# Optimization experiments

Measured on AMD Instinct MI355X. Metric: run time of the kernel, lower is better.

## Reference

```python
import jax, jax.numpy as jnp
import numpy as np

D = 256
H = 8
DH = D // H
N_NODES = 2048
N_EDGES = 4096
NEG = -10000.0
LN_EPS = 1e-5


def _layernorm(x, g, b):
    mu = jnp.mean(x, axis=-1, keepdims=True)
    var = jnp.var(x, axis=-1, keepdims=True)
    return (x - mu) * jax.lax.rsqrt(var + LN_EPS) * g + b


def setup_inputs() -> dict:
    key = jax.random.key(0)
    ks = jax.random.split(key, 20)
    s = 0.05
    x = jax.random.normal(ks[0], (N_NODES, D), jnp.float32)
    edge_index = jax.random.randint(ks[1], (2, N_EDGES), 0, N_NODES)
    edge_attr = jax.random.normal(ks[2], (N_EDGES, D), jnp.float32)
    edge_masks = jax.random.bernoulli(ks[3], 0.95, (N_EDGES, N_EDGES))
    return {
        "x": x,
        "edge_index": edge_index,
        "edge_attr": edge_attr,
        "edge_masks": edge_masks,
        # message MLP: Linear(3d, d) -> LeakyReLU(0.2) -> Linear(d, d)
        "W1": jax.random.normal(ks[4], (D, 3 * D), jnp.float32) * s,
        "b1": jnp.zeros((D,), jnp.float32),
        "W2": jax.random.normal(ks[5], (D, D), jnp.float32) * s,
        "b2": jnp.zeros((D,), jnp.float32),
        # MultiheadAttention params
        "in_proj_w": jax.random.normal(ks[6], (3 * D, D), jnp.float32) * s,
        "in_proj_b": jnp.zeros((3 * D,), jnp.float32),
        "out_w": jax.random.normal(ks[7], (D, D), jnp.float32) * s,
        "out_b": jnp.zeros((D,), jnp.float32),
        # GraphConv root weight + bias
        "root": jax.random.normal(ks[8], (D, D), jnp.float32) * s,
        "bias_p": jnp.zeros((D,), jnp.float32),
        # LayerNorms + residual linear
        "ln1_g": jnp.ones((D,), jnp.float32),
        "ln1_b": jnp.zeros((D,), jnp.float32),
        "ln2_g": jnp.ones((D,), jnp.float32),
        "ln2_b": jnp.zeros((D,), jnp.float32),
        "lin_w": jax.random.normal(ks[9], (D, D), jnp.float32) * s,
        "lin_b": jnp.zeros((D,), jnp.float32),
    }


def reference(x, edge_index, edge_attr, edge_masks,
              W1, b1, W2, b2,
              in_proj_w, in_proj_b, out_w, out_b,
              root, bias_p, ln1_g, ln1_b, ln2_g, ln2_b, lin_w, lin_b):
    # --- message: gather endpoints, concat with edge features, MLP ---
    x_j = x[edge_index[0]]            # source [E, d]
    x_i = x[edge_index[1]]            # target [E, d]
    h = jnp.concatenate([x_i, x_j, edge_attr], axis=1)          # [E, 3d]
    h = jax.nn.leaky_relu(h @ W1.T + b1, negative_slope=0.2)
    h = h @ W2.T + b2                                            # [E, d]

    # --- MultiheadAttention over edges (L=E, batch=1), eval mode ---
    qkv = h @ in_proj_w.T + in_proj_b                            # [E, 3d]
    q, k, v = jnp.split(qkv, 3, axis=1)
    q = q.reshape(N_EDGES, H, DH).transpose(1, 0, 2)             # [H, E, dh]
    k = k.reshape(N_EDGES, H, DH).transpose(1, 0, 2)
    v = v.reshape(N_EDGES, H, DH).transpose(1, 0, 2)
    scores = jnp.einsum('hed,hfd->hef', q, k) / np.sqrt(DH)      # [H, E, E]
    add_mask = jnp.where(edge_masks, 0.0, NEG).astype(scores.dtype)
    attn = jax.nn.softmax(scores + add_mask[None], axis=-1)
    o = jnp.einsum('hef,hfd->hed', attn, v)                      # [H, E, dh]
    o = o.transpose(1, 0, 2).reshape(N_EDGES, D)
    msg = o @ out_w.T + out_b                                    # [E, d]

    # --- scatter-add aggregation to target nodes + update ---
    aggr = jax.ops.segment_sum(msg, edge_index[1], num_segments=N_NODES)
    out = aggr + x @ root + bias_p                               # [N, d]

    # --- graph_block: norm1 -> residual linear -> norm2 ---
    y = _layernorm(out, ln1_g, ln1_b)
    y = _layernorm(y + (y @ lin_w.T + lin_b), ln2_g, ln2_b)
    return y
```

## Files before the change

### kernel.cpp

```cpp
#include <hip/hip_runtime.h>
#include <hip/hip_bf16.h>
#include <cstdint>

#define D_   256
#define E_   4096
#define NN_  2048

typedef float f32x4_t __attribute__((ext_vector_type(4)));
typedef short bf16x8_t __attribute__((ext_vector_type(8)));
typedef short bf16x4_t __attribute__((ext_vector_type(4)));

__device__ inline short f2bf(float f) {
    union { float fv; unsigned u; } v; v.fv = f;
    unsigned r = v.u + 0x7fffu + ((v.u >> 16) & 1u);
    return (short)(r >> 16);
}

__device__ inline unsigned cvtpk_bf16(float lo, float hi) {
    unsigned r;
    asm("v_cvt_pk_bf16_f32 %0, %1, %2" : "=v"(r) : "v"(lo), "v"(hi));
    return r;
}

__device__ inline float hw_exp2(float x) {
    float r;
    asm("v_exp_f32 %0, %1" : "=v"(r) : "v"(x));
    return r;
}

template<int ACT, bool GATHER, bool SCATTER, bool HASADD, bool ABF16, int OUT>
__global__ __launch_bounds__(256)
void mgemm_k(const void* __restrict__ A, const float* __restrict__ Bm,
             const float* __restrict__ bias, const float* __restrict__ addsrc,
             void* __restrict__ C, short* __restrict__ vtb,
             int M, int N, int K,
             const int* __restrict__ ei0, const int* __restrict__ ei1,
             const float* __restrict__ x, const float* __restrict__ eattr,
             float qsc)
{
    __shared__ char lds[16384];
    const int tid = threadIdx.x;
    const int w = tid >> 6, l = tid & 63;
    const int g = l >> 4, ln = l & 15;
    const int wr = w >> 1, wc = w & 1;
    const int m0 = blockIdx.x * 64, n0 = blockIdx.y * 64;

    const int srow = tid >> 2;
    const int sck  = (tid & 3) * 8;
    const int sswz = (srow & 7) << 4;
    int gi1 = 0, gi0 = 0;
    if (GATHER) { gi1 = ei1[m0 + srow]; gi0 = ei0[m0 + srow]; }

    f32x4_t acc[2][2];
    #pragma unroll
    for (int m = 0; m < 2; m++)
        #pragma unroll
        for (int n = 0; n < 2; n++)
            acc[m][n] = f32x4_t{0.f, 0.f, 0.f, 0.f};

    const int nt = K >> 5;
    float4 ga0, ga1, gb0, gb1;
    bf16x8_t gab;

    auto loadG = [&](int kk) {
        const int cb = kk + sck;
        if (ABF16) {
            gab = *(const bf16x8_t*)((const short*)A + (size_t)(m0 + srow) * K + cb);
        } else {
            const float* src;
            if (GATHER) {
                if (cb < 256)      src = x + (size_t)gi1 * 256 + cb;
                else if (cb < 512) src = x + (size_t)gi0 * 256 + (cb - 256);
                else               src = eattr + (size_t)(m0 + srow) * 256 + (cb - 512);
            } else {
                src = (const float*)A + (size_t)(m0 + srow) * K + cb;
            }
            ga0 = *(const float4*)src;
            ga1 = *(const float4*)(src + 4);
        }
        const float* bsrc = Bm + (size_t)(n0 + srow) * K + cb;
        gb0 = *(const float4*)bsrc;
        gb1 = *(const float4*)(bsrc + 4);
    };
    auto writeS = [&](int buf) {
        const int off = (srow*64 + sck*2) ^ sswz;
        if (ABF16) {
            *(bf16x8_t*)(lds + buf*4096 + off) = gab;
        } else {
            uint4 pa;
            pa.x = cvtpk_bf16(ga0.x, ga0.y); pa.y = cvtpk_bf16(ga0.z, ga0.w);
            pa.z = cvtpk_bf16(ga1.x, ga1.y); pa.w = cvtpk_bf16(ga1.z, ga1.w);
            *(uint4*)(lds + buf*4096 + off) = pa;
        }
        uint4 pb;
        pb.x = cvtpk_bf16(gb0.x, gb0.y); pb.y = cvtpk_bf16(gb0.z, gb0.w);
        pb.z = cvtpk_bf16(gb1.x, gb1.y); pb.w = cvtpk_bf16(gb1.z, gb1.w);
        *(uint4*)(lds + 8192 + buf*4096 + off) = pb;
    };

    loadG(0);
    writeS(0);
    __syncthreads();
    int cur = 0;
    for (int t = 0; t < nt; ++t) {
        if (t + 1 < nt) loadG((t + 1) << 5);
        bf16x8_t af[2], bfr[2];
        #pragma unroll
        for (int m = 0; m < 2; m++) {
            const int row = wr*32 + m*16 + ln;
            af[m] = *(const bf16x8_t*)(lds + cur*4096 + ((row*64 + g*16) ^ ((row&7)<<4)));
        }
        #pragma unroll
        for (int n = 0; n < 2; n++) {
            const int row = wc*32 + n*16 + ln;
            bfr[n] = *(const bf16x8_t*)(lds + 8192 + cur*4096 + ((row*64 + g*16) ^ ((row&7)<<4)));
        }
        #pragma unroll
        for (int m = 0; m < 2; m++)
            #pragma unroll
            for (int n = 0; n < 2; n++)
                acc[m][n] = __builtin_amdgcn_mfma_f32_16x16x32_bf16(af[m], bfr[n], acc[m][n], 0, 0, 0);
        if (t + 1 < nt) writeS(cur ^ 1);
        __syncthreads();
        cur ^= 1;
    }

    #pragma unroll
    for (int m = 0; m < 2; m++) {
        #pragma unroll
        for (int n = 0; n < 2; n++) {
            const int col = n0 + wc*32 + n*16 + ln;
            const float bv = bias[col];
            const int row0 = m0 + wr*32 + m*16 + g*4;
            float pv[4];
            #pragma unroll
            for (int r = 0; r < 4; r++) {
                float v = acc[m][n][r] + bv;
                if (ACT == 1) v = v > 0.f ? v : 0.2f * v;
                if (HASADD) v += addsrc[(size_t)(row0 + r) * N + col];
                pv[r] = v;
            }
            if (SCATTER) {
                #pragma unroll
                for (int r = 0; r < 4; r++)
                    atomicAdd(&((float*)C)[(size_t)ei1[row0 + r] * 256 + col], pv[r]);
            } else if (OUT == 0) {
                #pragma unroll
                for (int r = 0; r < 4; r++)
                    ((float*)C)[(size_t)(row0 + r) * N + col] = pv[r];
            } else if (OUT == 1) {
                #pragma unroll
                for (int r = 0; r < 4; r++)
                    ((short*)C)[(size_t)(row0 + r) * N + col] =
                        f2bf((col < 256) ? pv[r] * qsc : pv[r]);
            } else {
                if (col < 512) {
                    #pragma unroll
                    for (int r = 0; r < 4; r++)
                        ((short*)C)[(size_t)(row0 + r) * 768 + col] =
                            f2bf((col < 256) ? pv[r] * qsc : pv[r]);
                } else {
                    const int hd = (col - 512) >> 5, d = (col - 512) & 31;
                    bf16x4_t pk;
                    #pragma unroll
                    for (int r = 0; r < 4; r++) pk[r] = f2bf(pv[r]);
                    *(bf16x4_t*)(vtb + (size_t)hd*131072 + (size_t)d*4096 + row0) = pk;
                }
            }
        }
    }
}

__global__ __launch_bounds__(256)
void prep_k(const int* __restrict__ mraw, unsigned int* __restrict__ pm,
            const float* __restrict__ root, float* __restrict__ rootT,
            float* __restrict__ aggr)
{
    __shared__ float T[64][65];
    const int bid = blockIdx.x;
    if (bid < 2048) {
        const int t = bid * 256 + threadIdx.x;
        aggr[t] = 0.f;
        const int row = t >> 7, wb = t & 127;
        unsigned int bits = 0;
        const uint4* p = (const uint4*)(mraw + (size_t)row * 4096 + wb * 32);
        #pragma unroll
        for (int g = 0; g < 8; g++) {
            const uint4 v = p[g];
            if (v.x) bits |= 1u << (g*4+0);
            if (v.y) bits |= 1u << (g*4+1);
            if (v.z) bits |= 1u << (g*4+2);
            if (v.w) bits |= 1u << (g*4+3);
        }
        pm[t] = bits;
    } else {
        const int bt = bid - 2048;
        const int m0 = (bt >> 2) * 64, n0 = (bt & 3) * 64;
        const int r = threadIdx.x >> 6, c = threadIdx.x & 63;
        #pragma unroll
        for (int i = 0; i < 16; i++)
            T[r + i*4][c] = root[(size_t)(m0 + r + i*4) * 256 + n0 + c];
        __syncthreads();
        #pragma unroll
        for (int i = 0; i < 16; i++)
            rootT[(size_t)(n0 + r + i*4) * 256 + m0 + c] = T[c][r + i*4];
    }
}

__global__ __launch_bounds__(512, 4)
void attn_k(const short* __restrict__ qkvb, const short* __restrict__ vt,
            const unsigned int* __restrict__ pmask, float* __restrict__ o)
{
    __shared__ char lds[49152];
    const int tid = threadIdx.x;
    const int w2 = tid >> 6, l = tid & 63;
    const int g = l >> 4, ln = l & 15;
    const int gi = w2 >> 2, wq = w2 & 3;
    const int head = blockIdx.x >> 6;
    const int q0 = (blockIdx.x & 63) * 64;
    const int qa = q0 + wq * 16 + ln;

    const bf16x8_t qf = *(const bf16x8_t*)(qkvb + (size_t)qa*768 + head*32 + g*8);

    f32x4_t oT0 = {0.f,0.f,0.f,0.f};
    f32x4_t oT1 = {0.f,0.f,0.f,0.f};
    float lsum = 0.f;

    const int st = tid & 255;
    const int skey = st >> 2, sc = st & 3;
    const int sd = st >> 3, skc = st & 7;
    const short* kgp = qkvb + 256 + head*32 + sc*8;
    const short* vgp = vt + (size_t)head*131072 + (size_t)sd*4096 + skc*8;
    char* Kg = lds + gi*8192;
    char* Vg = lds + 16384 + gi*8192;
    char* Pw = lds + 32768 + w2*2048;
    const unsigned int* mrow = pmask + (size_t)qa*128;
    const int kswz = (skey & 7) << 4, vswz = (sd & 7) << 4;
    const int pswz = (ln & 7) << 4;

    uint2 mwc;
    {
        const int k0 = gi * 64;
        const bf16x8_t kv = *(const bf16x8_t*)(kgp + (size_t)(k0 + skey)*768);
        *(bf16x8_t*)(Kg + ((skey*64 + sc*16) ^ kswz)) = kv;
        const bf16x8_t vv = *(const bf16x8_t*)(vgp + k0);
        *(bf16x8_t*)(Vg + ((sd*128 + skc*16) ^ vswz)) = vv;
        mwc = *(const uint2*)(mrow + gi*2);
    }

    for (int i = 0; i < 32; ++i) {
        __syncthreads();
        const int cur = i & 1;
        const int tt = 2*i + gi;
        uint2 mwn;
        if (i < 31) {
            const int k0n = (tt + 2) * 64;
            const bf16x8_t kv = *(const bf16x8_t*)(kgp + (size_t)(k0n + skey)*768);
            *(bf16x8_t*)(Kg + (cur^1)*4096 + ((skey*64 + sc*16) ^ kswz)) = kv;
            const bf16x8_t vv = *(const bf16x8_t*)(vgp + k0n);
            *(bf16x8_t*)(Vg + (cur^1)*4096 + ((sd*128 + skc*16) ^ vswz)) = vv;
            mwn = *(const uint2*)(mrow + (tt + 2)*2);
        }
        char* Kb = Kg + cur*4096;
        char* Vb = Vg + cur*4096;

        f32x4_t s[4];
        __builtin_amdgcn_s_setprio(1);
        #pragma unroll
        for (int kt = 0; kt < 4; kt++) {
            const int key = kt*16 + ln;
            const bf16x8_t kf = *(const bf16x8_t*)(Kb + ((key*64 + g*16) ^ ((key & 7) << 4)));
            f32x4_t z = {0.f,0.f,0.f,0.f};
            s[kt] = __builtin_amdgcn_mfma_f32_16x16x32_bf16(kf, qf, z, 0, 0, 0);
        }
        __builtin_amdgcn_s_setprio(0);

        #pragma unroll
        for (int kt = 0; kt < 4; kt++) {
            const unsigned word = (kt < 2) ? mwc.x : mwc.y;
            float p[4];
            #pragma unroll
            for (int r = 0; r < 4; r++) {
                const float e = hw_exp2(s[kt][r] - 17.312340490667562f);
                p[r] = ((word >> ((kt & 1)*16 + g*4 + r)) & 1u) ? e : 0.f;
            }
            lsum += (p[0] + p[1]) + (p[2] + p[3]);
            uint2 pk;
            pk.x = cvtpk_bf16(p[0], p[1]);
            pk.y = cvtpk_bf16(p[2], p[3]);
            *(uint2*)(Pw + ((ln*128 + kt*32 + g*8) ^ pswz)) = pk;
        }

        __builtin_amdgcn_s_setprio(1);
        #pragma unroll
        for (int kh = 0; kh < 2; kh++) {
            const bf16x8_t pf = *(const bf16x8_t*)(Pw + ((ln*128 + kh*64 + g*16) ^ pswz));
            const bf16x8_t vf0 = *(const bf16x8_t*)(Vb + ((ln*128 + kh*64 + g*16) ^ pswz));
            const bf16x8_t vf1 = *(const bf16x8_t*)(Vb + (((16+ln)*128 + kh*64 + g*16) ^ pswz));
            oT0 = __builtin_amdgcn_mfma_f32_16x16x32_bf16(vf0, pf, oT0, 0, 0, 0);
            oT1 = __builtin_amdgcn_mfma_f32_16x16x32_bf16(vf1, pf, oT1, 0, 0, 0);
        }
        __builtin_amdgcn_s_setprio(0);
        mwc = mwn;
    }

    __syncthreads();
    *(f32x4_t*)(lds + w2*2048 + l*32)      = oT0;
    *(f32x4_t*)(lds + w2*2048 + l*32 + 16) = oT1;
    ((float*)(lds + 16384))[w2*64 + l] = lsum;
    __syncthreads();
    if (gi == 0) {
        const int pw = w2 + 4;
        const f32x4_t b0 = *(const f32x4_t*)(lds + pw*2048 + l*32);
        const f32x4_t b1 = *(const f32x4_t*)(lds + pw*2048 + l*32 + 16);
        const float lp = ((const float*)(lds + 16384))[pw*64 + l];
        oT0 += b0; oT1 += b1;
        lsum += lp;
        lsum += __shfl_xor(lsum, 16);
        lsum += __shfl_xor(lsum, 32);
        const float inv = 1.0f / fmaxf(lsum, 1e-37f);
        float* op = o + (size_t)qa * 256 + head*32;
        float4 v0 = {oT0[0]*inv, oT0[1]*inv, oT0[2]*inv, oT0[3]*inv};
        float4 v1 = {oT1[0]*inv, oT1[1]*inv, oT1[2]*inv, oT1[3]*inv};
        *(float4*)(op + g*4) = v0;
        *(float4*)(op + 16 + g*4) = v1;
    }
}

__global__ __launch_bounds__(256)
void ln_k(const float* __restrict__ in, const float* __restrict__ g,
          const float* __restrict__ b, float* __restrict__ out)
{
    const int n = blockIdx.x, t = threadIdx.x;
    const float v = in[(size_t)n * 256 + t];
    float s1 = v, s2 = v * v;
    #pragma unroll
    for (int off = 32; off > 0; off >>= 1) {
        s1 += __shfl_xor(s1, off);
        s2 += __shfl_xor(s2, off);
    }
    __shared__ float r1[4], r2[4];
    const int wv = t >> 6;
    if ((t & 63) == 0) { r1[wv] = s1; r2[wv] = s2; }
    __syncthreads();
    const float t1 = r1[0] + r1[1] + r1[2] + r1[3];
    const float t2 = r2[0] + r2[1] + r2[2] + r2[3];
    const float mu  = t1 * (1.0f / 256.0f);
    const float var = t2 * (1.0f / 256.0f) - mu * mu;
    const float rs  = rsqrtf(var + 1e-5f);
    out[(size_t)n * 256 + t] = (v - mu) * rs * g[t] + b[t];
}

extern "C" void kernel_launch(void* const* d_in, const int* in_sizes, int n_in,
                              void* d_out, int out_size, void* d_ws, size_t ws_size,
                              hipStream_t stream)
{
    const float* x     = (const float*)d_in[0];
    const int*   ei    = (const int*)  d_in[1];
    const float* eattr = (const float*)d_in[2];
    const int*   mask  = (const int*)  d_in[3];
    const float* W1   = (const float*)d_in[4];
    const float* b1   = (const float*)d_in[5];
    const float* W2   = (const float*)d_in[6];
    const float* b2   = (const float*)d_in[7];
    const float* ipw  = (const float*)d_in[8];
    const float* ipb  = (const float*)d_in[9];
    const float* ow   = (const float*)d_in[10];
    const float* ob   = (const float*)d_in[11];
    const float* root = (const float*)d_in[12];
    const float* bp   = (const float*)d_in[13];
    const float* ln1g = (const float*)d_in[14];
    const float* ln1b = (const float*)d_in[15];
    const float* ln2g = (const float*)d_in[16];
    const float* ln2b = (const float*)d_in[17];
    const float* linw = (const float*)d_in[18];
    const float* linb = (const float*)d_in[19];
    const int* ei0 = ei;
    const int* ei1 = ei + E_;

    float* ws = (float*)d_ws;
    short* h1b   = (short*)ws;
    short* hb    = (short*)(ws + 524288);
    float* o     = ws + 1048576;
    float* y1    = ws + 1048576;
    float* z     = ws + 1572864;
    short* qkvb  = (short*)(ws + 2097152);
    float* aggr  = ws + 3670016;
    float* outb  = ws + 4194304;
    unsigned int* pmask = (unsigned int*)(ws + 4718592);
    short* vt    = (short*)(ws + 5242896);
    float* rootT = ws + 5767184;

    dim3 blk(256);
    prep_k<<<dim3(2064), blk, 0, stream>>>(mask, pmask, root, rootT, aggr);

    mgemm_k<1,true,false,false,false,1><<<dim3(64,4), blk, 0, stream>>>(
        nullptr, W1, b1, nullptr, h1b, nullptr, E_, 256, 768, ei0, ei1, x, eattr, 1.0f);
    mgemm_k<0,false,false,false,true,1><<<dim3(64,4), blk, 0, stream>>>(
        h1b, W2, b2, nullptr, hb, nullptr, E_, 256, 256, nullptr, nullptr, nullptr, nullptr, 1.0f);
    mgemm_k<0,false,false,false,true,2><<<dim3(64,12), blk, 0, stream>>>(
        hb, ipw, ipb, nullptr, qkvb, vt, E_, 768, 256, nullptr, nullptr, nullptr, nullptr,
        0.25503486f);
    attn_k<<<dim3(512), dim3(512), 0, stream>>>(qkvb, vt, pmask, o);
    mgemm_k<0,false,true,false,false,0><<<dim3(64,4), blk, 0, stream>>>(
        o, ow, ob, nullptr, aggr, nullptr, E_, 256, 256, nullptr, ei1, nullptr, nullptr, 1.0f);
    mgemm_k<0,false,false,true,false,0><<<dim3(32,4), blk, 0, stream>>>(
        x, rootT, bp, aggr, outb, nullptr, NN_, 256, 256, nullptr, nullptr, nullptr, nullptr, 1.0f);
    ln_k<<<dim3(2048), blk, 0, stream>>>(outb, ln1g, ln1b, y1);
    mgemm_k<0,false,false,true,false,0><<<dim3(32,4), blk, 0, stream>>>(
        y1, linw, linb, y1, z, nullptr, NN_, 256, 256, nullptr, nullptr, nullptr, nullptr, 1.0f);
    ln_k<<<dim3(2048), blk, 0, stream>>>(z, ln2g, ln2b, (float*)d_out);
}
```

Baseline: 122.2 us.

## Use 8-wave GEMM blocks with a 64-deep K tile and 16x32 per-wave outputs

The shared MFMA GEMM kernel now runs 512 threads (8 waves) instead of 256 on the same 64x64 output tile. Each wave computes a 16x32 sub-tile instead of 32x32. The K step doubles to 64, so LDS buffers double to 32 KB and there are half as many loop iterations and barriers. The aim is better latency hiding and fewer synchronisations for these small GEMMs. In exchange, each wave reuses A fragments less and the block uses more LDS and registers, which can lower how many blocks fit per CU.

```diff
diff --git a/kernel.cpp b/kernel.cpp
--- a/kernel.cpp
+++ b/kernel.cpp
@@ -29,7 +29,7 @@
 }
 
 template<int ACT, bool GATHER, bool SCATTER, bool HASADD, bool ABF16, int OUT>
-__global__ __launch_bounds__(256)
+__global__ __launch_bounds__(512)
 void mgemm_k(const void* __restrict__ A, const float* __restrict__ Bm,
              const float* __restrict__ bias, const float* __restrict__ addsrc,
              void* __restrict__ C, short* __restrict__ vtb,
@@ -38,28 +38,25 @@
              const float* __restrict__ x, const float* __restrict__ eattr,
              float qsc)
 {
-    __shared__ char lds[16384];
+    __shared__ char lds[32768];
     const int tid = threadIdx.x;
     const int w = tid >> 6, l = tid & 63;
     const int g = l >> 4, ln = l & 15;
     const int wr = w >> 1, wc = w & 1;
     const int m0 = blockIdx.x * 64, n0 = blockIdx.y * 64;
 
-    const int srow = tid >> 2;
-    const int sck  = (tid & 3) * 8;
+    const int srow = tid >> 3;
+    const int sck  = (tid & 7) * 8;
     const int sswz = (srow & 7) << 4;
     int gi1 = 0, gi0 = 0;
     if (GATHER) { gi1 = ei1[m0 + srow]; gi0 = ei0[m0 + srow]; }
 
-    f32x4_t acc[2][2];
-    #pragma unroll
-    for (int m = 0; m < 2; m++)
-        #pragma unroll
-        for (int n = 0; n < 2; n++)
-            acc[m][n] = f32x4_t{0.f, 0.f, 0.f, 0.f};
-
-    const int nt = K >> 5;
-    float4 ga0, ga1, gb0, gb1;
+    f32x4_t acc[2];
+    acc[0] = f32x4_t{0.f,0.f,0.f,0.f};
+    acc[1] = f32x4_t{0.f,0.f,0.f,0.f};
+
+    const int nt = K >> 6;
+    float4 ga[2], gb[2];
     bf16x8_t gab;
 
     auto loadG = [&](int kk) {
@@ -75,27 +72,27 @@
             } else {
                 src = (const float*)A + (size_t)(m0 + srow) * K + cb;
             }
-            ga0 = *(const float4*)src;
-            ga1 = *(const float4*)(src + 4);
+            ga[0] = *(const float4*)src;
+            ga[1] = *(const float4*)(src + 4);
         }
         const float* bsrc = Bm + (size_t)(n0 + srow) * K + cb;
-        gb0 = *(const float4*)bsrc;
-        gb1 = *(const float4*)(bsrc + 4);
+        gb[0] = *(const float4*)bsrc;
+        gb[1] = *(const float4*)(bsrc + 4);
     };
     auto writeS = [&](int buf) {
-        const int off = (srow*64 + sck*2) ^ sswz;
+        const int off = (srow*128 + sck*2) ^ sswz;
         if (ABF16) {
-            *(bf16x8_t*)(lds + buf*4096 + off) = gab;
+            *(bf16x8_t*)(lds + buf*8192 + off) = gab;
         } else {
             uint4 pa;
-            pa.x = cvtpk_bf16(ga0.x, ga0.y); pa.y = cvtpk_bf16(ga0.z, ga0.w);
-            pa.z = cvtpk_bf16(ga1.x, ga1.y); pa.w = cvtpk_bf16(ga1.z, ga1.w);
-            *(uint4*)(lds + buf*4096 + off) = pa;
+            pa.x = cvtpk_bf16(ga[0].x, ga[0].y); pa.y = cvtpk_bf16(ga[0].z, ga[0].w);
+            pa.z = cvtpk_bf16(ga[1].x, ga[1].y); pa.w = cvtpk_bf16(ga[1].z, ga[1].w);
+            *(uint4*)(lds + buf*8192 + off) = pa;
         }
         uint4 pb;
-        pb.x = cvtpk_bf16(gb0.x, gb0.y); pb.y = cvtpk_bf16(gb0.z, gb0.w);
-        pb.z = cvtpk_bf16(gb1.x, gb1.y); pb.w = cvtpk_bf16(gb1.z, gb1.w);
-        *(uint4*)(lds + 8192 + buf*4096 + off) = pb;
+        pb.x = cvtpk_bf16(gb[0].x, gb[0].y); pb.y = cvtpk_bf16(gb[0].z, gb[0].w);
+        pb.z = cvtpk_bf16(gb[1].x, gb[1].y); pb.w = cvtpk_bf16(gb[1].z, gb[1].w);
+        *(uint4*)(lds + 16384 + buf*8192 + off) = pb;
     };
 
     loadG(0);
@@ -103,69 +100,63 @@
     __syncthreads();
     int cur = 0;
     for (int t = 0; t < nt; ++t) {
-        if (t + 1 < nt) loadG((t + 1) << 5);
-        bf16x8_t af[2], bfr[2];
-        #pragma unroll
-        for (int m = 0; m < 2; m++) {
-            const int row = wr*32 + m*16 + ln;
-            af[m] = *(const bf16x8_t*)(lds + cur*4096 + ((row*64 + g*16) ^ ((row&7)<<4)));
-        }
-        #pragma unroll
-        for (int n = 0; n < 2; n++) {
-            const int row = wc*32 + n*16 + ln;
-            bfr[n] = *(const bf16x8_t*)(lds + 8192 + cur*4096 + ((row*64 + g*16) ^ ((row&7)<<4)));
-        }
-        #pragma unroll
-        for (int m = 0; m < 2; m++)
+        if (t + 1 < nt) loadG((t + 1) << 6);
+        #pragma unroll
+        for (int kc = 0; kc < 2; kc++) {
+            const int arow = wr*16 + ln;
+            const bf16x8_t af = *(const bf16x8_t*)(lds + cur*8192 +
+                    ((arow*128 + kc*64 + g*16) ^ ((arow&7)<<4)));
             #pragma unroll
-            for (int n = 0; n < 2; n++)
-                acc[m][n] = __builtin_amdgcn_mfma_f32_16x16x32_bf16(af[m], bfr[n], acc[m][n], 0, 0, 0);
+            for (int n = 0; n < 2; n++) {
+                const int brow = wc*32 + n*16 + ln;
+                const bf16x8_t bfr = *(const bf16x8_t*)(lds + 16384 + cur*8192 +
+                         ((brow*128 + kc*64 + g*16) ^ ((brow&7)<<4)));
+                acc[n] = __builtin_amdgcn_mfma_f32_16x16x32_bf16(af, bfr, acc[n], 0, 0, 0);
+            }
+        }
         if (t + 1 < nt) writeS(cur ^ 1);
         __syncthreads();
         cur ^= 1;
     }
 
     #pragma unroll
-    for (int m = 0; m < 2; m++) {
-        #pragma unroll
-        for (int n = 0; n < 2; n++) {
-            const int col = n0 + wc*32 + n*16 + ln;
-            const float bv = bias[col];
-            const int row0 = m0 + wr*32 + m*16 + g*4;
-            float pv[4];
+    for (int n = 0; n < 2; n++) {
+        const int col = n0 + wc*32 + n*16 + ln;
+        const float bv = bias[col];
+        const int row0 = m0 + wr*16 + g*4;
+        float pv[4];
+        #pragma unroll
+        for (int r = 0; r < 4; r++) {
+            float v = acc[n][r] + bv;
+            if (ACT == 1) v = v > 0.f ? v : 0.2f * v;
+            if (HASADD) v += addsrc[(size_t)(row0 + r) * N + col];
+            pv[r] = v;
+        }
+        if (SCATTER) {
             #pragma unroll
-            for (int r = 0; r < 4; r++) {
-                float v = acc[m][n][r] + bv;
-                if (ACT == 1) v = v > 0.f ? v : 0.2f * v;
-                if (HASADD) v += addsrc[(size_t)(row0 + r) * N + col];
-                pv[r] = v;
-            }
-            if (SCATTER) {
+            for (int r = 0; r < 4; r++)
+                atomicAdd(&((float*)C)[(size_t)ei1[row0 + r] * 256 + col], pv[r]);
+        } else if (OUT == 0) {
+            #pragma unroll
+            for (int r = 0; r < 4; r++)
+                ((float*)C)[(size_t)(row0 + r) * N + col] = pv[r];
+        } else if (OUT == 1) {
+            #pragma unroll
+            for (int r = 0; r < 4; r++)
+                ((short*)C)[(size_t)(row0 + r) * N + col] =
+                    f2bf((col < 256) ? pv[r] * qsc : pv[r]);
+        } else {
+            if (col < 512) {
                 #pragma unroll
                 for (int r = 0; r < 4; r++)
-                    atomicAdd(&((float*)C)[(size_t)ei1[row0 + r] * 256 + col], pv[r]);
-            } else if (OUT == 0) {
-                #pragma unroll
-                for (int r = 0; r < 4; r++)
-                    ((float*)C)[(size_t)(row0 + r) * N + col] = pv[r];
-            } else if (OUT == 1) {
-                #pragma unroll
-                for (int r = 0; r < 4; r++)
-                    ((short*)C)[(size_t)(row0 + r) * N + col] =
+                    ((short*)C)[(size_t)(row0 + r) * 768 + col] =
                         f2bf((col < 256) ? pv[r] * qsc : pv[r]);
             } else {
-                if (col < 512) {
-                    #pragma unroll
-                    for (int r = 0; r < 4; r++)
-                        ((short*)C)[(size_t)(row0 + r) * 768 + col] =
-                            f2bf((col < 256) ? pv[r] * qsc : pv[r]);
-                } else {
-                    const int hd = (col - 512) >> 5, d = (col - 512) & 31;
-                    bf16x4_t pk;
-                    #pragma unroll
-                    for (int r = 0; r < 4; r++) pk[r] = f2bf(pv[r]);
-                    *(bf16x4_t*)(vtb + (size_t)hd*131072 + (size_t)d*4096 + row0) = pk;
-                }
+                const int hd = (col - 512) >> 5, d = (col - 512) & 31;
+                bf16x4_t pk;
+                #pragma unroll
+                for (int r = 0; r < 4; r++) pk[r] = f2bf(pv[r]);
+                *(bf16x4_t*)(vtb + (size_t)hd*131072 + (size_t)d*4096 + row0) = pk;
             }
         }
     }
@@ -392,22 +383,23 @@
     float* rootT = ws + 5767184;
 
     dim3 blk(256);
+    dim3 blk512(512);
     prep_k<<<dim3(2064), blk, 0, stream>>>(mask, pmask, root, rootT, aggr);
 
-    mgemm_k<1,true,false,false,false,1><<<dim3(64,4), blk, 0, stream>>>(
+    mgemm_k<1,true,false,false,false,1><<<dim3(64,4), blk512, 0, stream>>>(
         nullptr, W1, b1, nullptr, h1b, nullptr, E_, 256, 768, ei0, ei1, x, eattr, 1.0f);
-    mgemm_k<0,false,false,false,true,1><<<dim3(64,4), blk, 0, stream>>>(
+    mgemm_k<0,false,false,false,true,1><<<dim3(64,4), blk512, 0, stream>>>(
         h1b, W2, b2, nullptr, hb, nullptr, E_, 256, 256, nullptr, nullptr, nullptr, nullptr, 1.0f);
-    mgemm_k<0,false,false,false,true,2><<<dim3(64,12), blk, 0, stream>>>(
+    mgemm_k<0,false,false,false,true,2><<<dim3(64,12), blk512, 0, stream>>>(
         hb, ipw, ipb, nullptr, qkvb, vt, E_, 768, 256, nullptr, nullptr, nullptr, nullptr,
         0.25503486f);
     attn_k<<<dim3(512), dim3(512), 0, stream>>>(qkvb, vt, pmask, o);
-    mgemm_k<0,false,true,false,false,0><<<dim3(64,4), blk, 0, stream>>>(
+    mgemm_k<0,false,true,false,false,0><<<dim3(64,4), blk512, 0, stream>>>(
         o, ow, ob, nullptr, aggr, nullptr, E_, 256, 256, nullptr, ei1, nullptr, nullptr, 1.0f);
-    mgemm_k<0,false,false,true,false,0><<<dim3(32,4), blk, 0, stream>>>(
+    mgemm_k<0,false,false,true,false,0><<<dim3(32,4), blk512, 0, stream>>>(
         x, rootT, bp, aggr, outb, nullptr, NN_, 256, 256, nullptr, nullptr, nullptr, nullptr, 1.0f);
     ln_k<<<dim3(2048), blk, 0, stream>>>(outb, ln1g, ln1b, y1);
-    mgemm_k<0,false,false,true,false,0><<<dim3(32,4), blk, 0, stream>>>(
+    mgemm_k<0,false,false,true,false,0><<<dim3(32,4), blk512, 0, stream>>>(
         y1, linw, linb, y1, z, nullptr, NN_, 256, 256, nullptr, nullptr, nullptr, nullptr, 1.0f);
     ln_k<<<dim3(2048), blk, 0, stream>>>(z, ln2g, ln2b, (float*)d_out);
 }
```

Result: faster. 110.6 us (-9.5%).
